# Optimization experiments

Hardware: AMD Instinct MI355X
Metric: run time of the kernel (lower is better)

The kernel has to match this reference:

```python
import jax, jax.numpy as jnp
import numpy as np

# Dimensions inferred from the module (few-shot reweighted YOLOv2 region loss)
B, C, NA, NCPA = 64, 20, 5, 1          # batch, base classes, anchors, classes-per-anchor
H, W = 19, 19                           # feature map (608 input / stride 32)
T = 50                                  # cfg.max_boxes
THRESH = 0.6
COORD_SCALE = 1.0
CLASS_SCALE = 1.0
NB = B * C                              # per-class 'image' rows, as in the torch code
A4 = NA * H * W
EPS = 1e-12
BCE_EPS = 1e-7
ANCHORS = [[1.3221, 1.73145], [3.19275, 4.00944], [5.05587, 8.09892], [9.47112, 4.84053], [11.2364, 10.0071]]


def iou_xywh(x1, y1, w1, h1, x2, y2, w2, h2):
    # center-size IoU, matches darknet bbox_iou(x1y1x2y2=False)
    l = jnp.maximum(x1 - w1 * 0.5, x2 - w2 * 0.5)
    r = jnp.minimum(x1 + w1 * 0.5, x2 + w2 * 0.5)
    t = jnp.maximum(y1 - h1 * 0.5, y2 - h2 * 0.5)
    b = jnp.minimum(y1 + h1 * 0.5, y2 + h2 * 0.5)
    inter = jnp.clip(r - l, 0.0) * jnp.clip(b - t, 0.0)
    union = w1 * h1 + w2 * h2 - inter
    return inter / jnp.maximum(union, EPS)


def setup_inputs() -> dict:
    key = jax.random.key(0)
    k1, k2, k3, k4 = jax.random.split(key, 4)
    output = jax.random.normal(k1, (NB, NA * (5 + NCPA), H, W), jnp.float32) * 0.5
    # target rows: [cls, x, y, w, h] * T, coords in (0,1); x kept > 0 so all boxes are 'valid'
    cls_ids = jax.random.randint(k2, (B, C, T), 0, C).astype(jnp.float32)
    xy = jax.random.uniform(k3, (B, C, T, 2), minval=0.05, maxval=0.95)
    wh = jax.random.uniform(k4, (B, C, T, 2), minval=0.05, maxval=0.5)
    target = jnp.concatenate([cls_ids[..., None], xy, wh], axis=-1).reshape(B, C, T * 5)
    anchors = jnp.asarray(ANCHORS, jnp.float32)
    return {"output": output, "target": target, "anchors": anchors}


def _forward(output, target, anchors):
    target = jax.lax.stop_gradient(target)
    anchors = jax.lax.stop_gradient(anchors)
    out5 = output.reshape(NB, NA, 5 + NCPA, H, W)
    x = jax.nn.sigmoid(out5[:, :, 0])
    y = jax.nn.sigmoid(out5[:, :, 1])
    w = out5[:, :, 2]
    h = out5[:, :, 3]
    conf = jax.nn.sigmoid(out5[:, :, 4])
    # class logits regrouped to original batch: (B*NA*H*W, C)
    cls = out5[:, :, 5:5 + NCPA].reshape(NB, NA, H, W)
    cls_logits = cls.reshape(B, C, NA * H * W).transpose(0, 2, 1).reshape(-1, C)
    # decode pred boxes (detached, mirroring torch's use of .data)
    grid_x = jnp.arange(W, dtype=jnp.float32)[None, None, None, :]
    grid_y = jnp.arange(H, dtype=jnp.float32)[None, None, :, None]
    aw = anchors[:, 0][None, :, None, None]
    ah = anchors[:, 1][None, :, None, None]
    px = jax.lax.stop_gradient(x) + grid_x
    py = jax.lax.stop_gradient(y) + grid_y
    pw = jnp.exp(jax.lax.stop_gradient(w)) * aw
    ph = jnp.exp(jax.lax.stop_gradient(h)) * ah
    # ground-truth boxes per row
    tgt = target.reshape(NB, T, 5)
    cls_t = tgt[:, :, 0]
    gx = tgt[:, :, 1] * W
    gy = tgt[:, :, 2] * H
    gw = tgt[:, :, 3] * W
    gh = tgt[:, :, 4] * H
    # 'break on first zero x' semantics
    valid = jnp.cumprod((tgt[:, :, 1] != 0).astype(jnp.int32), axis=1) > 0
    # stage 1: zero conf_mask where any gt IoU > thresh (scan over T to avoid (NB,T,A4) blowup)
    pxf = px.reshape(NB, A4); pyf = py.reshape(NB, A4)
    pwf = pw.reshape(NB, A4); phf = ph.reshape(NB, A4)

    def iou_step(ci, xs):
        gxt, gyt, gwt, ght, vt = xs
        iou = iou_xywh(pxf, pyf, pwf, phf, gxt[:, None], gyt[:, None], gwt[:, None], ght[:, None])
        return jnp.maximum(ci, jnp.where(vt[:, None], iou, 0.0)), None

    cur_ious, _ = jax.lax.scan(iou_step, jnp.zeros((NB, A4), jnp.float32), (gx.T, gy.T, gw.T, gh.T, valid.T))
    conf_mask0 = jnp.where(cur_ious.reshape(NB, NA, H, W) > THRESH, 0.0, 1.0)
    # best anchor per gt by wh-only IoU
    inter = jnp.minimum(gw[..., None], anchors[:, 0]) * jnp.minimum(gh[..., None], anchors[:, 1])
    union = gw[..., None] * gh[..., None] + anchors[:, 0] * anchors[:, 1] - inter
    best_n = jnp.argmax(inter / jnp.maximum(union, EPS), axis=-1).astype(jnp.int32)  # (NB,T)
    gi = gx.astype(jnp.int32)
    gj = gy.astype(jnp.int32)
    # stage 2: ordered scatter of targets (later boxes overwrite earlier, as in the torch loops)
    binds = jnp.arange(NB)
    z = jnp.zeros((NB, NA, H, W), jnp.float32)
    # seen < 12800 branch: tx=ty=0.5, tw=th=0, coord_mask=1
    carry0 = (jnp.ones_like(z), z, conf_mask0, jnp.full_like(z, 0.5), jnp.full_like(z, 0.5), z, z, z, z)

    def tgt_step(carry, xs):
        cm, clm, cfm, tx, ty, tw, th, tconf, tcls = carry
        gxt, gyt, gwt, ght, bn, git, gjt, vt, ct = xs
        idx = (binds, bn, gjt, git)

        def upd(arr, val):
            return arr.at[idx].set(jnp.where(vt, val, arr[idx]))

        aw_b = anchors[bn, 0]
        ah_b = anchors[bn, 1]
        iou = iou_xywh(gxt, gyt, gwt, ght, px[idx], py[idx], pw[idx], ph[idx])
        cm = upd(cm, 1.0)
        clm = upd(clm, 1.0)
        cfm = upd(cfm, 1.0)
        tx = upd(tx, gxt - git.astype(jnp.float32))
        ty = upd(ty, gyt - gjt.astype(jnp.float32))
        tw = upd(tw, jnp.log(jnp.maximum(gwt, EPS) / aw_b))
        th = upd(th, jnp.log(jnp.maximum(ght, EPS) / ah_b))
        tconf = upd(tconf, iou)
        tcls = upd(tcls, ct)
        return (cm, clm, cfm, tx, ty, tw, th, tconf, tcls), None

    xs = (gx.T, gy.T, gw.T, gh.T, best_n.T, gi.T, gj.T, valid.T, cls_t.T)
    (coord_mask, cls_mask, conf_mask, tx, ty, tw, th, tconf, tcls), _ = jax.lax.scan(tgt_step, carry0, xs)
    # regroup per-class rows back to original batch (neg_ratio='full' -> counts[i] == C)
    cm_grp = cls_mask.reshape(B, C, NA, H, W).sum(axis=1)
    tcls_grp = tcls.reshape(B, C, NA, H, W).sum(axis=1)
    sel = (cm_grp == 1.0).reshape(-1)           # exclude colliding cells
    labels = tcls_grp.reshape(-1).astype(jnp.int32)

    def bce_mean(p, t):
        p = jnp.clip(p, BCE_EPS, 1.0 - BCE_EPS)
        return jnp.mean(-(t * jnp.log(p) + (1.0 - t) * jnp.log(1.0 - p)))

    loss_x = COORD_SCALE * bce_mean(x * coord_mask, tx * coord_mask)
    loss_y = COORD_SCALE * bce_mean(y * coord_mask, ty * coord_mask)
    loss_w = COORD_SCALE * 0.5 * jnp.mean((w * coord_mask - tw * coord_mask) ** 2)
    loss_h = COORD_SCALE * 0.5 * jnp.mean((h * coord_mask - th * coord_mask) ** 2)
    loss_conf = 0.5 * jnp.mean((conf * conf_mask - tconf * conf_mask) ** 2)
    logp = jax.nn.log_softmax(cls_logits, axis=-1)
    nll = -jnp.take_along_axis(logp, labels[:, None], axis=1)[:, 0]
    nsel = jnp.maximum(jnp.sum(sel.astype(jnp.float32)), 1.0)
    loss_cls = CLASS_SCALE * jnp.sum(jnp.where(sel, nll, 0.0)) / nsel
    return loss_x + loss_y + loss_w + loss_h + loss_conf + loss_cls


def reference(output, target, anchors):
    return _forward(output, target, anchors)
```

## Files before the change

kernel.cpp:

```cpp
#include <hip/hip_runtime.h>
#include <math.h>

constexpr int cB   = 64;
constexpr int cC   = 20;
constexpr int cNA  = 5;
constexpr int cH   = 19;
constexpr int cW   = 19;
constexpr int cT   = 50;
constexpr int cNB  = cB * cC;
constexpr int cHW  = cH * cW;
constexpr int cA4  = cNA * cHW;
constexpr int cCH  = cNA * 6;
constexpr long cNTOT = (long)cNB * cA4;
constexpr int cCLS_BLOCKS = cB * cNA;

__device__ __constant__ float cAW[cNA]   = {1.3221f, 3.19275f, 5.05587f, 9.47112f, 11.2364f};
__device__ __constant__ float cAH[cNA]   = {1.73145f, 4.00944f, 8.09892f, 4.84053f, 10.0071f};
__device__ __constant__ float cAREA[cNA] = {2.28930345f, 12.80114796f, 40.94706183f, 45.84455262f, 112.44377644f};
__device__ __constant__ float cLNAW[cNA] = {0.27920469f, 1.16088088f, 1.62060702f, 2.24822684f, 2.41915174f};
__device__ __constant__ float cLNAH[cNA] = {0.54896100f, 1.38865236f, 2.09173157f, 1.57701337f, 2.30329495f};

constexpr int ACC_BANKS = 64;
constexpr size_t OFF_CNT = 2560;
constexpr size_t OFF_ROW = 4096;
constexpr size_t ZERO_BYTES = OFF_ROW + (size_t)cB * cA4 * 4;
constexpr int    ZERO_INT4  = (int)(ZERO_BYTES / 16);
constexpr size_t OFF_GB4 = 466432;
constexpr size_t OFF_GB1 = OFF_GB4 + (size_t)cNB * cT * 16;
constexpr size_t WS_NEEDED = OFF_GB1 + (size_t)cNB * cT * 4;

__device__ __forceinline__ float fexp(float x) {
    return __builtin_amdgcn_exp2f(x * 1.4426950408889634f);
}
__device__ __forceinline__ float flog(float x) {
    return __builtin_amdgcn_logf(x) * 0.6931471805599453f;
}
__device__ __forceinline__ float frcp(float x) { return __builtin_amdgcn_rcpf(x); }

typedef _Float16 h2 __attribute__((ext_vector_type(2)));
union HU { unsigned u; h2 h; };
__device__ __forceinline__ unsigned splat2(float v) {
    HU x; _Float16 f = (_Float16)v; x.h[0] = f; x.h[1] = f; return x.u;
}
constexpr float cS = 1.2649110640673518f;

__launch_bounds__(256)
__global__ void k_init(const float* __restrict__ target, int4* __restrict__ wsz,
                       uint4* __restrict__ gb4, unsigned* __restrict__ gb1) {
    const int gtid = blockIdx.x * 256 + threadIdx.x;
    int4 z4; z4.x = z4.y = z4.z = z4.w = 0;
    for (int k = gtid; k < ZERO_INT4; k += cCLS_BLOCKS * 256) wsz[k] = z4;

    const int nb = blockIdx.x * 4 + (threadIdx.x >> 6);
    const int t  = threadIdx.x & 63;
    float xr = 1.f, yr = 0.f, wr = 0.f, hr = 0.f;
    const bool isT = (t < cT);
    if (isT) {
        const float* tg = target + (size_t)nb * (cT * 5) + t * 5;
        xr = tg[1]; yr = tg[2]; wr = tg[3]; hr = tg[4];
    }
    unsigned long long nz = __ballot(xr != 0.0f);
    if (isT) {
        unsigned long long below = (2ull << t) - 1ull;
        bool valid = ((~nz) & below) == 0ull;
        const int idx = nb * cT + t;
        float gx = xr * (float)cW, gy = yr * (float)cH;
        float gw = wr * (float)cW, gh = hr * (float)cH;
        uint4 bx;
        if (valid) {
            bx.x = splat2(cS * (gx - 0.5f * gw));
            bx.y = splat2(cS * (gx + 0.5f * gw));
            bx.z = splat2(cS * (gy - 0.5f * gh));
            bx.w = splat2(cS * (gy + 0.5f * gh));
            gb1[idx] = splat2(-0.6f * (gw * gh));
        } else {
            bx.x = splat2(1e4f);  bx.y = splat2(-1e4f);
            bx.z = splat2(1e4f);  bx.w = splat2(-1e4f);
            gb1[idx] = splat2(0.0f);
        }
        gb4[idx] = bx;
    }
}

template<bool GB>
__launch_bounds__(256)
__global__ void k_main(const float* __restrict__ outp, const float* __restrict__ target,
                       const uint4* __restrict__ gb4, const unsigned* __restrict__ gb1,
                       int* __restrict__ rowenc, double* __restrict__ acc) {
    __shared__ int s_win[1024];
    __shared__ float4 s_gt[cT];
    __shared__ __align__(16) unsigned s_box[GB ? 1 : cT][8];
    __shared__ double s_red[3][4];
    const int tid  = threadIdx.x;
    const int swz  = ((int)(blockIdx.x & 7)) * 320 + ((int)blockIdx.x >> 3);
    const int nb   = swz >> 1;
    const int half = swz & 1;
    const int winoff = half << 10;
    const int base = winoff + tid;
    const int b_   = nb / cC;
    const int c_   = nb - b_ * cC;
    const float* obase = outp + (size_t)nb * (cCH * cHW);
    const int nbT = nb * cT;

    s_win[tid] = -1; s_win[tid + 256] = -1;
    s_win[tid + 512] = -1; s_win[tid + 768] = -1;
    __syncthreads();

    int myCell = -1;
    if (tid < 64) {
        const int t = tid;
        float xr = 1.f, yr = 0.f, wr = 0.f, hr = 0.f;
        if (t < cT) {
            const float* tg = target + (size_t)nb * (cT * 5) + t * 5;
            xr = tg[1]; yr = tg[2]; wr = tg[3]; hr = tg[4];
        }
        unsigned long long nz = __ballot(xr != 0.0f);
        if (t < cT) {
            unsigned long long below = (2ull << t) - 1ull;
            bool valid = ((~nz) & below) == 0ull;
            float gx = xr * (float)cW, gy = yr * (float)cH;
            float gw = wr * (float)cW, gh = hr * (float)cH;
            s_gt[t] = make_float4(gx, gy, gw, gh);
            if (valid) {
                float garea = gw * gh;
                float best = -1.0f; int bn = 0;
                for (int n = 0; n < cNA; ++n) {
                    float inter = fminf(gw, cAW[n]) * fminf(gh, cAH[n]);
                    float uni   = garea + cAREA[n] - inter;
                    float r = inter / fmaxf(uni, 1e-12f);
                    if (r > best) { best = r; bn = n; }
                }
                int cell = bn * cHW + (int)gy * cW + (int)gx;
                myCell = cell;
                if constexpr (!GB) {
                    s_box[t][0] = splat2(cS * (gx - 0.5f * gw));
                    s_box[t][1] = splat2(cS * (gx + 0.5f * gw));
                    s_box[t][2] = splat2(cS * (gy - 0.5f * gh));
                    s_box[t][3] = splat2(cS * (gy + 0.5f * gh));
                    s_box[t][4] = splat2(-0.6f * garea);
                }
                if (cell >= winoff && cell < winoff + 1024)
                    atomicMax(&s_win[cell - winoff], t);
            } else if constexpr (!GB) {
                s_box[t][0] = splat2(1e4f);  s_box[t][1] = splat2(-1e4f);
                s_box[t][2] = splat2(1e4f);  s_box[t][3] = splat2(-1e4f);
                s_box[t][4] = splat2(0.0f);
            }
        }
    }
    __syncthreads();
    if (tid < cT && myCell >= winoff && myCell < winoff + 1024 &&
        s_win[myCell - winoff] == tid)
        atomicAdd(&rowenc[b_ * cA4 + myCell], (1 << 10) | (c_ * cT + tid));

    h2 pl2[2], pr2[2], pt2[2], pb2[2], ov2[2], pa06h[2];
    float conf[4], tcf[4];
    unsigned wbits = 0;
    float bce = 0.0f, sq = 0.0f;
    const h2 z2 = { (_Float16)0.0f, (_Float16)0.0f };
    constexpr float cLN2 = 0.6931471805599453f;

    #pragma unroll
    for (int u = 0; u < 4; ++u) {
        int cell = base + (u << 8);
        bool a_  = cell < cA4;
        int cc   = a_ ? cell : (cA4 - 1);
        int na   = cc / cHW;
        int rem  = cc - na * cHW;
        int j    = rem / cW;
        int i    = rem - j * cW;
        const float* ob = obase + (size_t)(na * 6) * cHW + rem;
        float xl = ob[0], yl = ob[cHW], wl = ob[2*cHW], hl = ob[3*cHW], cl = ob[4*cHW];
        float Ex = __builtin_amdgcn_exp2f(-1.4426950408889634f * xl);
        float Sx = 1.0f + Ex;
        float x  = frcp(Sx);
        float Lx = __builtin_amdgcn_logf(Sx);
        float Ey = __builtin_amdgcn_exp2f(-1.4426950408889634f * yl);
        float Sy = 1.0f + Ey;
        float y  = frcp(Sy);
        float Ly = __builtin_amdgcn_logf(Sy);
        float cf = frcp(1.0f + fexp(-cl));
        float px = x + (float)i, py = y + (float)j;
        float pw = fexp(wl) * cAW[na], ph = fexp(hl) * cAH[na];
        float l0 = px - 0.5f*pw, r0 = px + 0.5f*pw;
        float t0 = py - 0.5f*ph, b0 = py + 0.5f*ph;
        float pa = pw * ph;
        int p = u >> 1, s = u & 1;
        pl2[p][s] = (_Float16)(cS * l0);  pr2[p][s] = (_Float16)(cS * r0);
        pt2[p][s] = (_Float16)(cS * t0);  pb2[p][s] = (_Float16)(cS * b0);
        pa06h[p][s] = (_Float16)(0.6f * pa);
        ov2[p][s] = (_Float16)0.0f;
        conf[u] = cf;

        float tx = 0.5f, ty = 0.5f, tw = 0.0f, th = 0.0f, tc = 0.0f;
        int wt = s_win[cc - winoff];
        bool wfl = (wt >= 0) && a_;
        if (wfl) {
            wbits |= (1u << u);
            float4 g = s_gt[wt];
            tx = g.x - (float)i;  ty = g.y - (float)j;
            tw = flog(fmaxf(g.z, 1e-12f)) - cLNAW[na];
            th = flog(fmaxf(g.w, 1e-12f)) - cLNAH[na];
            float iw = fminf(r0, g.x + 0.5f*g.z) - fmaxf(l0, g.x - 0.5f*g.z);
            float ih = fminf(b0, g.y + 0.5f*g.w) - fmaxf(t0, g.y - 0.5f*g.w);
            iw = fmaxf(iw, 0.0f); ih = fmaxf(ih, 0.0f);
            float inter = iw * ih;
            float uni   = g.z * g.w + pa - inter;
            tc = inter * frcp(fmaxf(uni, 1e-12f));
        }
        tcf[u] = tc;
        if (a_) {
            bce += (1.0f - tx) * xl + cLN2 * Lx;
            bce += (1.0f - ty) * yl + cLN2 * Ly;
            float dw = wl - tw, dh = hl - th;
            sq += dw*dw + dh*dh;
        }
    }

    #pragma unroll 10
    for (int t = 0; t < cT; ++t) {
        unsigned w0, w1, w2, w3, w4;
        if constexpr (GB) {
            uint4 bx = gb4[nbT + t];
            w0 = bx.x; w1 = bx.y; w2 = bx.z; w3 = bx.w;
            w4 = gb1[nbT + t];
        } else {
            uint4 bx = *(const uint4*)&s_box[t][0];
            w0 = bx.x; w1 = bx.y; w2 = bx.z; w3 = bx.w;
            w4 = s_box[t][4];
        }
        HU a, b, c, d, e;
        a.u = w0; b.u = w1; c.u = w2; d.u = w3; e.u = w4;
        #pragma unroll
        for (int p = 0; p < 2; ++p) {
            h2 iw = __builtin_elementwise_min(pr2[p], b.h) - __builtin_elementwise_max(pl2[p], a.h);
            h2 ih = __builtin_elementwise_min(pb2[p], d.h) - __builtin_elementwise_max(pt2[p], c.h);
            iw = __builtin_elementwise_max(iw, z2);
            ov2[p] = __builtin_elementwise_max(ov2[p], iw * ih + e.h);
        }
    }

    float sc = 0.0f;
    #pragma unroll
    for (int u = 0; u < 4; ++u) {
        int cell = base + (u << 8);
        if (cell >= cA4) continue;
        int p = u >> 1, s = u & 1;
        bool wfl  = (wbits >> u) & 1;
        bool over = ov2[p][s] > pa06h[p][s];
        float cm  = wfl ? 1.0f : (over ? 0.0f : 1.0f);
        float d   = (conf[u] - tcf[u]) * cm;
        sc += d * d;
    }

    double v0 = (double)bce, v1 = (double)sq, v2 = (double)sc;
    for (int off = 32; off > 0; off >>= 1) {
        v0 += __shfl_down(v0, off);
        v1 += __shfl_down(v1, off);
        v2 += __shfl_down(v2, off);
    }
    int lane = tid & 63, wid = tid >> 6;
    if (lane == 0) { s_red[0][wid] = v0; s_red[1][wid] = v1; s_red[2][wid] = v2; }
    __syncthreads();
    if (tid == 0) {
        double a0 = s_red[0][0] + s_red[0][1] + s_red[0][2] + s_red[0][3];
        double a1 = s_red[1][0] + s_red[1][1] + s_red[1][2] + s_red[1][3];
        double a2 = s_red[2][0] + s_red[2][1] + s_red[2][2] + s_red[2][3];
        int bank = blockIdx.x & (ACC_BANKS - 1);
        atomicAdd(&acc[0*ACC_BANKS + bank], a0);
        atomicAdd(&acc[1*ACC_BANKS + bank], a1);
        atomicAdd(&acc[2*ACC_BANKS + bank], a2);
    }
}

__launch_bounds__(384)
__global__ void k_cls(const float* __restrict__ outp, const float* __restrict__ target,
                      const int* __restrict__ rowenc, double* __restrict__ acc,
                      int* __restrict__ cnt, float* __restrict__ out) {
    __shared__ double s_red[2][6];
    __shared__ int s_last;
    const int tid = threadIdx.x;
    const int b   = blockIdx.x / cNA;
    const int na  = blockIdx.x - b * cNA;
    double nll = 0.0, ns = 0.0;
    if (tid < cHW) {
        const int rem = tid;
        const float* ob = outp + ((size_t)(b * cC) * cCH + na * 6 + 5) * cHW + rem;
        float l[cC]; float m = -1e30f;
        #pragma unroll
        for (int c = 0; c < cC; ++c) {
            l[c] = ob[(size_t)c * (cCH * cHW)];
            m = fmaxf(m, l[c]);
        }
        float s = 0.0f;
        #pragma unroll
        for (int c = 0; c < cC; ++c) s += fexp(l[c] - m);
        float lse = m + flog(s);
        int row = b * cA4 + na * cHW + rem;
        int v = rowenc[row];
        if ((v >> 10) == 1) {
            int payload = v & 1023;
            int selc = payload / cT;
            int selt = payload - selc * cT;
            int label = (int)target[((size_t)(b * cC + selc) * cT + selt) * 5];
            nll = (double)(lse - l[label]);
            ns  = 1.0;
        }
    }
    for (int off = 32; off > 0; off >>= 1) {
        nll += __shfl_down(nll, off);
        ns  += __shfl_down(ns, off);
    }
    int lane = tid & 63, wid = tid >> 6;
    if (lane == 0) { s_red[0][wid] = nll; s_red[1][wid] = ns; }
    __syncthreads();
    if (tid == 0) {
        double a0 = 0.0, a1 = 0.0;
        #pragma unroll
        for (int w = 0; w < 6; ++w) { a0 += s_red[0][w]; a1 += s_red[1][w]; }
        int bank = blockIdx.x & (ACC_BANKS - 1);
        atomicAdd(&acc[3*ACC_BANKS + bank], a0);
        atomicAdd(&acc[4*ACC_BANKS + bank], a1);
        __threadfence();
        s_last = (atomicAdd(cnt, 1) == cCLS_BLOCKS - 1);
    }
    __syncthreads();
    if (s_last && tid < 64) {
        __threadfence();
        double s[5];
        #pragma unroll
        for (int j = 0; j < 5; ++j) {
            double v = atomicAdd(&acc[j * ACC_BANKS + tid], 0.0);
            for (int off = 32; off > 0; off >>= 1) v += __shfl_down(v, off);
            s[j] = v;
        }
        if (tid == 0) {
            double Ninv = 1.0 / (double)cNTOT;
            double loss = s[0] * Ninv
                        + 0.5 * s[1] * Ninv
                        + 0.5 * s[2] * Ninv
                        + s[3] / fmax(s[4], 1.0);
            out[0] = (float)loss;
        }
    }
}

extern "C" void kernel_launch(void* const* d_in, const int* in_sizes, int n_in,
                              void* d_out, int out_size, void* d_ws, size_t ws_size,
                              hipStream_t stream) {
    const float* output = (const float*)d_in[0];
    const float* target = (const float*)d_in[1];
    char* ws = (char*)d_ws;
    double*   acc    = (double*)ws;
    int*      cnt    = (int*)(ws + OFF_CNT);
    int*      rowenc = (int*)(ws + OFF_ROW);
    uint4*    gb4    = (uint4*)(ws + OFF_GB4);
    unsigned* gb1    = (unsigned*)(ws + OFF_GB1);

    if (ws_size >= WS_NEEDED) {
        k_init<<<cCLS_BLOCKS, 256, 0, stream>>>(target, (int4*)ws, gb4, gb1);
        k_main<true><<<cNB * 2, 256, 0, stream>>>(output, target, gb4, gb1, rowenc, acc);
    } else {
        hipMemsetAsync(ws, 0, ZERO_BYTES, stream);
        k_main<false><<<cNB * 2, 256, 0, stream>>>(output, target, gb4, gb1, rowenc, acc);
    }
    k_cls<<<cCLS_BLOCKS, 384, 0, stream>>>(output, target, rowenc, acc, cnt, (float*)d_out);
}
```

Before: 126.6 us.

## Merge class-loss kernel into main kernel and compute cell winners locally

Drops the separate class-loss kernel and the global rowenc table. Class-loss blocks now recompute each target's best anchor cell per batch image, resolve collisions with wave shuffles, and record counts and labels in shared memory. These blocks run in the same launch as the main blocks, and the last block to finish reduces the accumulators. This removes one launch, the zeroing of the large rowenc buffer, and its global atomics, at the cost of redoing target-to-cell assignment in the class blocks.

```diff
diff --git a/kernel.cpp b/kernel.cpp
--- a/kernel.cpp
+++ b/kernel.cpp
@@ -12,7 +12,9 @@
 constexpr int cA4  = cNA * cHW;
 constexpr int cCH  = cNA * 6;
 constexpr long cNTOT = (long)cNB * cA4;
-constexpr int cCLS_BLOCKS = cB * cNA;
+constexpr int cCLS_BLOCKS  = cB * cNA;
+constexpr int cMAIN_BLOCKS = cNB * 2;
+constexpr int cALL_BLOCKS  = cCLS_BLOCKS + cMAIN_BLOCKS;
 
 __device__ __constant__ float cAW[cNA]   = {1.3221f, 3.19275f, 5.05587f, 9.47112f, 11.2364f};
 __device__ __constant__ float cAH[cNA]   = {1.73145f, 4.00944f, 8.09892f, 4.84053f, 10.0071f};
@@ -22,10 +24,7 @@
 
 constexpr int ACC_BANKS = 64;
 constexpr size_t OFF_CNT = 2560;
-constexpr size_t OFF_ROW = 4096;
-constexpr size_t ZERO_BYTES = OFF_ROW + (size_t)cB * cA4 * 4;
-constexpr int    ZERO_INT4  = (int)(ZERO_BYTES / 16);
-constexpr size_t OFF_GB4 = 466432;
+constexpr size_t OFF_GB4 = 4096;
 constexpr size_t OFF_GB1 = OFF_GB4 + (size_t)cNB * cT * 16;
 constexpr size_t WS_NEEDED = OFF_GB1 + (size_t)cNB * cT * 4;
 
@@ -44,12 +43,22 @@
 }
 constexpr float cS = 1.2649110640673518f;
 
+__device__ __forceinline__ int best_cell(float gx, float gy, float gw, float gh) {
+    float garea = gw * gh;
+    float best = -1.0f; int bn = 0;
+    for (int n = 0; n < cNA; ++n) {
+        float inter = fminf(gw, cAW[n]) * fminf(gh, cAH[n]);
+        float uni   = garea + cAREA[n] - inter;
+        float r = inter / fmaxf(uni, 1e-12f);
+        if (r > best) { best = r; bn = n; }
+    }
+    return bn * cHW + (int)gy * cW + (int)gx;
+}
+
 __launch_bounds__(256)
 __global__ void k_init(const float* __restrict__ target, int4* __restrict__ wsz,
                        uint4* __restrict__ gb4, unsigned* __restrict__ gb1) {
-    const int gtid = blockIdx.x * 256 + threadIdx.x;
-    int4 z4; z4.x = z4.y = z4.z = z4.w = 0;
-    for (int k = gtid; k < ZERO_INT4; k += cCLS_BLOCKS * 256) wsz[k] = z4;
+    if (blockIdx.x == 0) wsz[threadIdx.x] = int4{0, 0, 0, 0};
 
     const int nb = blockIdx.x * 4 + (threadIdx.x >> 6);
     const int t  = threadIdx.x & 63;
@@ -84,245 +93,265 @@
 
 template<bool GB>
 __launch_bounds__(256)
-__global__ void k_main(const float* __restrict__ outp, const float* __restrict__ target,
-                       const uint4* __restrict__ gb4, const unsigned* __restrict__ gb1,
-                       int* __restrict__ rowenc, double* __restrict__ acc) {
+__global__ void k_merged(const float* __restrict__ outp, const float* __restrict__ target,
+                         const uint4* __restrict__ gb4, const unsigned* __restrict__ gb1,
+                         double* __restrict__ acc, int* __restrict__ cnt,
+                         float* __restrict__ out) {
     __shared__ int s_win[1024];
     __shared__ float4 s_gt[cT];
     __shared__ __align__(16) unsigned s_box[GB ? 1 : cT][8];
+    __shared__ int s_cnt[cHW];
+    __shared__ int s_lab[cHW];
     __shared__ double s_red[3][4];
+    __shared__ int s_last;
     const int tid  = threadIdx.x;
-    const int swz  = ((int)(blockIdx.x & 7)) * 320 + ((int)blockIdx.x >> 3);
-    const int nb   = swz >> 1;
-    const int half = swz & 1;
-    const int winoff = half << 10;
-    const int base = winoff + tid;
-    const int b_   = nb / cC;
-    const int c_   = nb - b_ * cC;
-    const float* obase = outp + (size_t)nb * (cCH * cHW);
-    const int nbT = nb * cT;
-
-    s_win[tid] = -1; s_win[tid + 256] = -1;
-    s_win[tid + 512] = -1; s_win[tid + 768] = -1;
-    __syncthreads();
-
-    int myCell = -1;
-    if (tid < 64) {
-        const int t = tid;
-        float xr = 1.f, yr = 0.f, wr = 0.f, hr = 0.f;
-        if (t < cT) {
-            const float* tg = target + (size_t)nb * (cT * 5) + t * 5;
-            xr = tg[1]; yr = tg[2]; wr = tg[3]; hr = tg[4];
-        }
-        unsigned long long nz = __ballot(xr != 0.0f);
-        if (t < cT) {
-            unsigned long long below = (2ull << t) - 1ull;
-            bool valid = ((~nz) & below) == 0ull;
-            float gx = xr * (float)cW, gy = yr * (float)cH;
-            float gw = wr * (float)cW, gh = hr * (float)cH;
-            s_gt[t] = make_float4(gx, gy, gw, gh);
-            if (valid) {
-                float garea = gw * gh;
-                float best = -1.0f; int bn = 0;
-                for (int n = 0; n < cNA; ++n) {
-                    float inter = fminf(gw, cAW[n]) * fminf(gh, cAH[n]);
-                    float uni   = garea + cAREA[n] - inter;
-                    float r = inter / fmaxf(uni, 1e-12f);
-                    if (r > best) { best = r; bn = n; }
+    const int bid  = blockIdx.x;
+    const int lane = tid & 63;
+    const int wid  = tid >> 6;
+
+    if (bid < cCLS_BLOCKS) {
+        const int b  = bid / cNA;
+        const int na = bid - b * cNA;
+        for (int k = tid; k < cHW; k += 256) { s_cnt[k] = 0; s_lab[k] = 0; }
+        __syncthreads();
+
+        for (int c = wid; c < cC; c += 4) {
+            const int nb = b * cC + c;
+            float cid = 0.f, xr = 1.f, yr = 0.f, wr = 0.f, hr = 0.f;
+            if (lane < cT) {
+                const float* tg = target + (size_t)nb * (cT * 5) + lane * 5;
+                cid = tg[0]; xr = tg[1]; yr = tg[2]; wr = tg[3]; hr = tg[4];
+            }
+            unsigned long long nz = __ballot(xr != 0.0f);
+            int cellv = -2 - lane;
+            bool valid = false;
+            if (lane < cT) {
+                unsigned long long below = (2ull << lane) - 1ull;
+                valid = ((~nz) & below) == 0ull;
+                if (valid)
+                    cellv = best_cell(xr * (float)cW, yr * (float)cH,
+                                      wr * (float)cW, hr * (float)cH);
+            }
+            bool loser = false;
+            for (int i2 = 1; i2 < cT; ++i2) {
+                int ci = __shfl(cellv, i2, 64);
+                loser |= (i2 > lane) && (ci == cellv);
+            }
+            if (valid && !loser) {
+                int lo = cellv - na * cHW;
+                if (lo >= 0 && lo < cHW) {
+                    atomicAdd(&s_cnt[lo], 1);
+                    atomicAdd(&s_lab[lo], (int)cid);
                 }
-                int cell = bn * cHW + (int)gy * cW + (int)gx;
-                myCell = cell;
-                if constexpr (!GB) {
-                    s_box[t][0] = splat2(cS * (gx - 0.5f * gw));
-                    s_box[t][1] = splat2(cS * (gx + 0.5f * gw));
-                    s_box[t][2] = splat2(cS * (gy - 0.5f * gh));
-                    s_box[t][3] = splat2(cS * (gy + 0.5f * gh));
-                    s_box[t][4] = splat2(-0.6f * garea);
+            }
+        }
+        __syncthreads();
+
+        double nll = 0.0, ns = 0.0;
+        #pragma unroll
+        for (int pass = 0; pass < 2; ++pass) {
+            const int rem = tid + (pass << 8);
+            if (rem < cHW) {
+                const float* ob = outp + ((size_t)(b * cC) * cCH + na * 6 + 5) * cHW + rem;
+                float l[cC]; float m = -1e30f;
+                #pragma unroll
+                for (int c = 0; c < cC; ++c) {
+                    l[c] = ob[(size_t)c * (cCH * cHW)];
+                    m = fmaxf(m, l[c]);
                 }
-                if (cell >= winoff && cell < winoff + 1024)
-                    atomicMax(&s_win[cell - winoff], t);
-            } else if constexpr (!GB) {
-                s_box[t][0] = splat2(1e4f);  s_box[t][1] = splat2(-1e4f);
-                s_box[t][2] = splat2(1e4f);  s_box[t][3] = splat2(-1e4f);
-                s_box[t][4] = splat2(0.0f);
-            }
-        }
-    }
-    __syncthreads();
-    if (tid < cT && myCell >= winoff && myCell < winoff + 1024 &&
-        s_win[myCell - winoff] == tid)
-        atomicAdd(&rowenc[b_ * cA4 + myCell], (1 << 10) | (c_ * cT + tid));
-
-    h2 pl2[2], pr2[2], pt2[2], pb2[2], ov2[2], pa06h[2];
-    float conf[4], tcf[4];
-    unsigned wbits = 0;
-    float bce = 0.0f, sq = 0.0f;
-    const h2 z2 = { (_Float16)0.0f, (_Float16)0.0f };
-    constexpr float cLN2 = 0.6931471805599453f;
-
-    #pragma unroll
-    for (int u = 0; u < 4; ++u) {
-        int cell = base + (u << 8);
-        bool a_  = cell < cA4;
-        int cc   = a_ ? cell : (cA4 - 1);
-        int na   = cc / cHW;
-        int rem  = cc - na * cHW;
-        int j    = rem / cW;
-        int i    = rem - j * cW;
-        const float* ob = obase + (size_t)(na * 6) * cHW + rem;
-        float xl = ob[0], yl = ob[cHW], wl = ob[2*cHW], hl = ob[3*cHW], cl = ob[4*cHW];
-        float Ex = __builtin_amdgcn_exp2f(-1.4426950408889634f * xl);
-        float Sx = 1.0f + Ex;
-        float x  = frcp(Sx);
-        float Lx = __builtin_amdgcn_logf(Sx);
-        float Ey = __builtin_amdgcn_exp2f(-1.4426950408889634f * yl);
-        float Sy = 1.0f + Ey;
-        float y  = frcp(Sy);
-        float Ly = __builtin_amdgcn_logf(Sy);
-        float cf = frcp(1.0f + fexp(-cl));
-        float px = x + (float)i, py = y + (float)j;
-        float pw = fexp(wl) * cAW[na], ph = fexp(hl) * cAH[na];
-        float l0 = px - 0.5f*pw, r0 = px + 0.5f*pw;
-        float t0 = py - 0.5f*ph, b0 = py + 0.5f*ph;
-        float pa = pw * ph;
-        int p = u >> 1, s = u & 1;
-        pl2[p][s] = (_Float16)(cS * l0);  pr2[p][s] = (_Float16)(cS * r0);
-        pt2[p][s] = (_Float16)(cS * t0);  pb2[p][s] = (_Float16)(cS * b0);
-        pa06h[p][s] = (_Float16)(0.6f * pa);
-        ov2[p][s] = (_Float16)0.0f;
-        conf[u] = cf;
-
-        float tx = 0.5f, ty = 0.5f, tw = 0.0f, th = 0.0f, tc = 0.0f;
-        int wt = s_win[cc - winoff];
-        bool wfl = (wt >= 0) && a_;
-        if (wfl) {
-            wbits |= (1u << u);
-            float4 g = s_gt[wt];
-            tx = g.x - (float)i;  ty = g.y - (float)j;
-            tw = flog(fmaxf(g.z, 1e-12f)) - cLNAW[na];
-            th = flog(fmaxf(g.w, 1e-12f)) - cLNAH[na];
-            float iw = fminf(r0, g.x + 0.5f*g.z) - fmaxf(l0, g.x - 0.5f*g.z);
-            float ih = fminf(b0, g.y + 0.5f*g.w) - fmaxf(t0, g.y - 0.5f*g.w);
-            iw = fmaxf(iw, 0.0f); ih = fmaxf(ih, 0.0f);
-            float inter = iw * ih;
-            float uni   = g.z * g.w + pa - inter;
-            tc = inter * frcp(fmaxf(uni, 1e-12f));
-        }
-        tcf[u] = tc;
-        if (a_) {
-            bce += (1.0f - tx) * xl + cLN2 * Lx;
-            bce += (1.0f - ty) * yl + cLN2 * Ly;
-            float dw = wl - tw, dh = hl - th;
-            sq += dw*dw + dh*dh;
-        }
-    }
-
-    #pragma unroll 10
-    for (int t = 0; t < cT; ++t) {
-        unsigned w0, w1, w2, w3, w4;
-        if constexpr (GB) {
-            uint4 bx = gb4[nbT + t];
-            w0 = bx.x; w1 = bx.y; w2 = bx.z; w3 = bx.w;
-            w4 = gb1[nbT + t];
-        } else {
-            uint4 bx = *(const uint4*)&s_box[t][0];
-            w0 = bx.x; w1 = bx.y; w2 = bx.z; w3 = bx.w;
-            w4 = s_box[t][4];
-        }
-        HU a, b, c, d, e;
-        a.u = w0; b.u = w1; c.u = w2; d.u = w3; e.u = w4;
+                float s = 0.0f;
+                #pragma unroll
+                for (int c = 0; c < cC; ++c) s += fexp(l[c] - m);
+                float lse = m + flog(s);
+                if (s_cnt[rem] == 1) {
+                    nll += (double)(lse - l[s_lab[rem]]);
+                    ns  += 1.0;
+                }
+            }
+        }
+        for (int off = 32; off > 0; off >>= 1) {
+            nll += __shfl_down(nll, off);
+            ns  += __shfl_down(ns, off);
+        }
+        if (lane == 0) { s_red[0][wid] = nll; s_red[1][wid] = ns; }
+        __syncthreads();
+        if (tid == 0) {
+            double a0 = s_red[0][0] + s_red[0][1] + s_red[0][2] + s_red[0][3];
+            double a1 = s_red[1][0] + s_red[1][1] + s_red[1][2] + s_red[1][3];
+            int bank = bid & (ACC_BANKS - 1);
+            atomicAdd(&acc[3*ACC_BANKS + bank], a0);
+            atomicAdd(&acc[4*ACC_BANKS + bank], a1);
+        }
+    } else {
+        const int mbid = bid - cCLS_BLOCKS;
+        const int swz  = ((mbid & 7)) * 320 + (mbid >> 3);
+        const int nb   = swz >> 1;
+        const int half = swz & 1;
+        const int winoff = half << 10;
+        const int base = winoff + tid;
+        const float* obase = outp + (size_t)nb * (cCH * cHW);
+        const int nbT = nb * cT;
+
+        s_win[tid] = -1; s_win[tid + 256] = -1;
+        s_win[tid + 512] = -1; s_win[tid + 768] = -1;
+        __syncthreads();
+
+        if (tid < 64) {
+            const int t = tid;
+            float xr = 1.f, yr = 0.f, wr = 0.f, hr = 0.f;
+            if (t < cT) {
+                const float* tg = target + (size_t)nb * (cT * 5) + t * 5;
+                xr = tg[1]; yr = tg[2]; wr = tg[3]; hr = tg[4];
+            }
+            unsigned long long nz = __ballot(xr != 0.0f);
+            if (t < cT) {
+                unsigned long long below = (2ull << t) - 1ull;
+                bool valid = ((~nz) & below) == 0ull;
+                float gx = xr * (float)cW, gy = yr * (float)cH;
+                float gw = wr * (float)cW, gh = hr * (float)cH;
+                s_gt[t] = make_float4(gx, gy, gw, gh);
+                if (valid) {
+                    int cell = best_cell(gx, gy, gw, gh);
+                    if constexpr (!GB) {
+                        s_box[t][0] = splat2(cS * (gx - 0.5f * gw));
+                        s_box[t][1] = splat2(cS * (gx + 0.5f * gw));
+                        s_box[t][2] = splat2(cS * (gy - 0.5f * gh));
+                        s_box[t][3] = splat2(cS * (gy + 0.5f * gh));
+                        s_box[t][4] = splat2(-0.6f * (gw * gh));
+                    }
+                    if (cell >= winoff && cell < winoff + 1024)
+                        atomicMax(&s_win[cell - winoff], t);
+                } else if constexpr (!GB) {
+                    s_box[t][0] = splat2(1e4f);  s_box[t][1] = splat2(-1e4f);
+                    s_box[t][2] = splat2(1e4f);  s_box[t][3] = splat2(-1e4f);
+                    s_box[t][4] = splat2(0.0f);
+                }
+            }
+        }
+        __syncthreads();
+
+        h2 pl2[2], pr2[2], pt2[2], pb2[2], ov2[2], pa06h[2];
+        float conf[4], tcf[4];
+        unsigned wbits = 0;
+        float bce = 0.0f, sq = 0.0f;
+        const h2 z2 = { (_Float16)0.0f, (_Float16)0.0f };
+        constexpr float cLN2 = 0.6931471805599453f;
+
         #pragma unroll
-        for (int p = 0; p < 2; ++p) {
-            h2 iw = __builtin_elementwise_min(pr2[p], b.h) - __builtin_elementwise_max(pl2[p], a.h);
-            h2 ih = __builtin_elementwise_min(pb2[p], d.h) - __builtin_elementwise_max(pt2[p], c.h);
-            iw = __builtin_elementwise_max(iw, z2);
-            ov2[p] = __builtin_elementwise_max(ov2[p], iw * ih + e.h);
-        }
-    }
-
-    float sc = 0.0f;
-    #pragma unroll
-    for (int u = 0; u < 4; ++u) {
-        int cell = base + (u << 8);
-        if (cell >= cA4) continue;
-        int p = u >> 1, s = u & 1;
-        bool wfl  = (wbits >> u) & 1;
-        bool over = ov2[p][s] > pa06h[p][s];
-        float cm  = wfl ? 1.0f : (over ? 0.0f : 1.0f);
-        float d   = (conf[u] - tcf[u]) * cm;
-        sc += d * d;
-    }
-
-    double v0 = (double)bce, v1 = (double)sq, v2 = (double)sc;
-    for (int off = 32; off > 0; off >>= 1) {
-        v0 += __shfl_down(v0, off);
-        v1 += __shfl_down(v1, off);
-        v2 += __shfl_down(v2, off);
-    }
-    int lane = tid & 63, wid = tid >> 6;
-    if (lane == 0) { s_red[0][wid] = v0; s_red[1][wid] = v1; s_red[2][wid] = v2; }
-    __syncthreads();
+        for (int u = 0; u < 4; ++u) {
+            int cell = base + (u << 8);
+            bool a_  = cell < cA4;
+            int cc   = a_ ? cell : (cA4 - 1);
+            int na   = cc / cHW;
+            int rem  = cc - na * cHW;
+            int j    = rem / cW;
+            int i    = rem - j * cW;
+            const float* ob = obase + (size_t)(na * 6) * cHW + rem;
+            float xl = ob[0], yl = ob[cHW], wl = ob[2*cHW], hl = ob[3*cHW], cl = ob[4*cHW];
+            float Ex = __builtin_amdgcn_exp2f(-1.4426950408889634f * xl);
+            float Sx = 1.0f + Ex;
+            float x  = frcp(Sx);
+            float Lx = __builtin_amdgcn_logf(Sx);
+            float Ey = __builtin_amdgcn_exp2f(-1.4426950408889634f * yl);
+            float Sy = 1.0f + Ey;
+            float y  = frcp(Sy);
+            float Ly = __builtin_amdgcn_logf(Sy);
+            float cf = frcp(1.0f + fexp(-cl));
+            float px = x + (float)i, py = y + (float)j;
+            float pw = fexp(wl) * cAW[na], ph = fexp(hl) * cAH[na];
+            float l0 = px - 0.5f*pw, r0 = px + 0.5f*pw;
+            float t0 = py - 0.5f*ph, b0 = py + 0.5f*ph;
+            float pa = pw * ph;
+            int p = u >> 1, s = u & 1;
+            pl2[p][s] = (_Float16)(cS * l0);  pr2[p][s] = (_Float16)(cS * r0);
+            pt2[p][s] = (_Float16)(cS * t0);  pb2[p][s] = (_Float16)(cS * b0);
+            pa06h[p][s] = (_Float16)(0.6f * pa);
+            ov2[p][s] = (_Float16)0.0f;
+            conf[u] = cf;
+
+            float tx = 0.5f, ty = 0.5f, tw = 0.0f, th = 0.0f, tc = 0.0f;
+            int wt = s_win[cc - winoff];
+            bool wfl = (wt >= 0) && a_;
+            if (wfl) {
+                wbits |= (1u << u);
+                float4 g = s_gt[wt];
+                tx = g.x - (float)i;  ty = g.y - (float)j;
+                tw = flog(fmaxf(g.z, 1e-12f)) - cLNAW[na];
+                th = flog(fmaxf(g.w, 1e-12f)) - cLNAH[na];
+                float iw = fminf(r0, g.x + 0.5f*g.z) - fmaxf(l0, g.x - 0.5f*g.z);
+                float ih = fminf(b0, g.y + 0.5f*g.w) - fmaxf(t0, g.y - 0.5f*g.w);
+                iw = fmaxf(iw, 0.0f); ih = fmaxf(ih, 0.0f);
+                float inter = iw * ih;
+                float uni   = g.z * g.w + pa - inter;
+                tc = inter * frcp(fmaxf(uni, 1e-12f));
+            }
+            tcf[u] = tc;
+            if (a_) {
+                bce += (1.0f - tx) * xl + cLN2 * Lx;
+                bce += (1.0f - ty) * yl + cLN2 * Ly;
+                float dw = wl - tw, dh = hl - th;
+                sq += dw*dw + dh*dh;
+            }
+        }
+
+        #pragma unroll 10
+        for (int t = 0; t < cT; ++t) {
+            unsigned w0, w1, w2, w3, w4;
+            if constexpr (GB) {
+                uint4 bx = gb4[nbT + t];
+                w0 = bx.x; w1 = bx.y; w2 = bx.z; w3 = bx.w;
+                w4 = gb1[nbT + t];
+            } else {
+                uint4 bx = *(const uint4*)&s_box[t][0];
+                w0 = bx.x; w1 = bx.y; w2 = bx.z; w3 = bx.w;
+                w4 = s_box[t][4];
+            }
+            HU a, b, c, d, e;
+            a.u = w0; b.u = w1; c.u = w2; d.u = w3; e.u = w4;
+            #pragma unroll
+            for (int p = 0; p < 2; ++p) {
+                h2 iw = __builtin_elementwise_min(pr2[p], b.h) - __builtin_elementwise_max(pl2[p], a.h);
+                h2 ih = __builtin_elementwise_min(pb2[p], d.h) - __builtin_elementwise_max(pt2[p], c.h);
+                iw = __builtin_elementwise_max(iw, z2);
+                ov2[p] = __builtin_elementwise_max(ov2[p], iw * ih + e.h);
+            }
+        }
+
+        float sc = 0.0f;
+        #pragma unroll
+        for (int u = 0; u < 4; ++u) {
+            int cell = base + (u << 8);
+            if (cell >= cA4) continue;
+            int p = u >> 1, s = u & 1;
+            bool wfl  = (wbits >> u) & 1;
+            bool over = ov2[p][s] > pa06h[p][s];
+            float cm  = wfl ? 1.0f : (over ? 0.0f : 1.0f);
+            float d   = (conf[u] - tcf[u]) * cm;
+            sc += d * d;
+        }
+
+        double v0 = (double)bce, v1 = (double)sq, v2 = (double)sc;
+        for (int off = 32; off > 0; off >>= 1) {
+            v0 += __shfl_down(v0, off);
+            v1 += __shfl_down(v1, off);
+            v2 += __shfl_down(v2, off);
+        }
+        if (lane == 0) { s_red[0][wid] = v0; s_red[1][wid] = v1; s_red[2][wid] = v2; }
+        __syncthreads();
+        if (tid == 0) {
+            double a0 = s_red[0][0] + s_red[0][1] + s_red[0][2] + s_red[0][3];
+            double a1 = s_red[1][0] + s_red[1][1] + s_red[1][2] + s_red[1][3];
+            double a2 = s_red[2][0] + s_red[2][1] + s_red[2][2] + s_red[2][3];
+            int bank = bid & (ACC_BANKS - 1);
+            atomicAdd(&acc[0*ACC_BANKS + bank], a0);
+            atomicAdd(&acc[1*ACC_BANKS + bank], a1);
+            atomicAdd(&acc[2*ACC_BANKS + bank], a2);
+        }
+    }
+
     if (tid == 0) {
-        double a0 = s_red[0][0] + s_red[0][1] + s_red[0][2] + s_red[0][3];
-        double a1 = s_red[1][0] + s_red[1][1] + s_red[1][2] + s_red[1][3];
-        double a2 = s_red[2][0] + s_red[2][1] + s_red[2][2] + s_red[2][3];
-        int bank = blockIdx.x & (ACC_BANKS - 1);
-        atomicAdd(&acc[0*ACC_BANKS + bank], a0);
-        atomicAdd(&acc[1*ACC_BANKS + bank], a1);
-        atomicAdd(&acc[2*ACC_BANKS + bank], a2);
-    }
-}
-
-__launch_bounds__(384)
-__global__ void k_cls(const float* __restrict__ outp, const float* __restrict__ target,
-                      const int* __restrict__ rowenc, double* __restrict__ acc,
-                      int* __restrict__ cnt, float* __restrict__ out) {
-    __shared__ double s_red[2][6];
-    __shared__ int s_last;
-    const int tid = threadIdx.x;
-    const int b   = blockIdx.x / cNA;
-    const int na  = blockIdx.x - b * cNA;
-    double nll = 0.0, ns = 0.0;
-    if (tid < cHW) {
-        const int rem = tid;
-        const float* ob = outp + ((size_t)(b * cC) * cCH + na * 6 + 5) * cHW + rem;
-        float l[cC]; float m = -1e30f;
-        #pragma unroll
-        for (int c = 0; c < cC; ++c) {
-            l[c] = ob[(size_t)c * (cCH * cHW)];
-            m = fmaxf(m, l[c]);
-        }
-        float s = 0.0f;
-        #pragma unroll
-        for (int c = 0; c < cC; ++c) s += fexp(l[c] - m);
-        float lse = m + flog(s);
-        int row = b * cA4 + na * cHW + rem;
-        int v = rowenc[row];
-        if ((v >> 10) == 1) {
-            int payload = v & 1023;
-            int selc = payload / cT;
-            int selt = payload - selc * cT;
-            int label = (int)target[((size_t)(b * cC + selc) * cT + selt) * 5];
-            nll = (double)(lse - l[label]);
-            ns  = 1.0;
-        }
-    }
-    for (int off = 32; off > 0; off >>= 1) {
-        nll += __shfl_down(nll, off);
-        ns  += __shfl_down(ns, off);
-    }
-    int lane = tid & 63, wid = tid >> 6;
-    if (lane == 0) { s_red[0][wid] = nll; s_red[1][wid] = ns; }
-    __syncthreads();
-    if (tid == 0) {
-        double a0 = 0.0, a1 = 0.0;
-        #pragma unroll
-        for (int w = 0; w < 6; ++w) { a0 += s_red[0][w]; a1 += s_red[1][w]; }
-        int bank = blockIdx.x & (ACC_BANKS - 1);
-        atomicAdd(&acc[3*ACC_BANKS + bank], a0);
-        atomicAdd(&acc[4*ACC_BANKS + bank], a1);
         __threadfence();
-        s_last = (atomicAdd(cnt, 1) == cCLS_BLOCKS - 1);
+        s_last = (atomicAdd(cnt, 1) == cALL_BLOCKS - 1);
     }
     __syncthreads();
     if (s_last && tid < 64) {
@@ -353,16 +382,16 @@
     char* ws = (char*)d_ws;
     double*   acc    = (double*)ws;
     int*      cnt    = (int*)(ws + OFF_CNT);
-    int*      rowenc = (int*)(ws + OFF_ROW);
     uint4*    gb4    = (uint4*)(ws + OFF_GB4);
     unsigned* gb1    = (unsigned*)(ws + OFF_GB1);
 
     if (ws_size >= WS_NEEDED) {
         k_init<<<cCLS_BLOCKS, 256, 0, stream>>>(target, (int4*)ws, gb4, gb1);
-        k_main<true><<<cNB * 2, 256, 0, stream>>>(output, target, gb4, gb1, rowenc, acc);
+        k_merged<true><<<cALL_BLOCKS, 256, 0, stream>>>(output, target, gb4, gb1,
+                                                        acc, cnt, (float*)d_out);
     } else {
-        hipMemsetAsync(ws, 0, ZERO_BYTES, stream);
-        k_main<false><<<cNB * 2, 256, 0, stream>>>(output, target, gb4, gb1, rowenc, acc);
-    }
-    k_cls<<<cCLS_BLOCKS, 384, 0, stream>>>(output, target, rowenc, acc, cnt, (float*)d_out);
-}
+        hipMemsetAsync(ws, 0, 4096, stream);
+        k_merged<false><<<cALL_BLOCKS, 256, 0, stream>>>(output, target, gb4, gb1,
+                                                         acc, cnt, (float*)d_out);
+    }
+}
```

Result: slower. 185.8 us (+46.7%).
